# Kernel optimization log

Measured on AMD Instinct MI355X. Metric: run time of the kernel, lower is better.

Reference implementation:

```python
import jax, jax.numpy as jnp
import numpy as np

NUM_NODES = 100000
NUM_EDGES = 1600000
DIM = 64
NUM_LAYERS = 3


def setup_inputs() -> dict:
    key = jax.random.key(0)
    k1, k2 = jax.random.split(key)
    x = jax.random.normal(k1, (NUM_NODES, DIM), dtype=jnp.float32)
    adj_t = jax.random.randint(k2, (2, NUM_EDGES), 0, NUM_NODES, dtype=jnp.int64)
    return {"x": x, "adj_t": adj_t}


def reference(x, adj_t):
    n = x.shape[0]
    # undirected -> add reversed edges (adj_t_is_undirected=True path)
    edge_index = jnp.concatenate([adj_t, adj_t[::-1]], axis=1)  # [2, 2E]
    row, col = edge_index[0], edge_index[1]
    edge_weight = jnp.ones((row.shape[0],), dtype=x.dtype)
    # gcn_norm: D^-0.5 A D^-0.5 (degree computed by scatter over col)
    deg = jax.ops.segment_sum(edge_weight, col, num_segments=n)
    deg_inv_sqrt = jnp.where(deg > 0, jax.lax.rsqrt(deg), 0.0).astype(x.dtype)
    w = deg_inv_sqrt[row] * edge_weight * deg_inv_sqrt[col]  # [2E]
    outs = [x]
    for _ in range(NUM_LAYERS):
        # gather -> scale -> scatter_add (SpMM)
        msgs = w[:, None] * x[row]                     # [2E, D]
        x = jax.ops.segment_sum(msgs, col, num_segments=n)  # [N, D]
        outs.append(x)
    return jnp.mean(jnp.stack(outs), axis=0)
```

## Files before the change

### kernel.cpp

```cpp
#include <hip/hip_runtime.h>

#define DIM 64
#define SCAN_B 256
#define BKT_SHIFT 7
#define BKT_G 128
#define NBLK 256
#define HIST_B 1024

__device__ inline float blo(unsigned p) { return __uint_as_float(p << 16); }
__device__ inline float bhi(unsigned p) { return __uint_as_float(p & 0xffff0000u); }
__device__ inline unsigned bpack(float x, float y) {
    unsigned ux = __float_as_uint(x);
    unsigned uy = __float_as_uint(y);
    ux += 0x7fffu + ((ux >> 16) & 1u);
    uy += 0x7fffu + ((uy >> 16) & 1u);
    return (ux >> 16) | (uy & 0xffff0000u);
}

__global__ __launch_bounds__(HIST_B)
void hist_kernel(const int* __restrict__ adj, int E,
                 int* __restrict__ hist, int NB) {
    extern __shared__ int lh[];
    for (int g = threadIdx.x; g < NB; g += blockDim.x) lh[g] = 0;
    __syncthreads();
    for (int e = blockIdx.x * blockDim.x + threadIdx.x; e < E;
         e += NBLK * blockDim.x) {
        int a = adj[e];
        int b = adj[E + e];
        atomicAdd(&lh[a >> BKT_SHIFT], 1);
        atomicAdd(&lh[b >> BKT_SHIFT], 1);
    }
    __syncthreads();
    for (int g = threadIdx.x; g < NB; g += blockDim.x)
        hist[g * NBLK + blockIdx.x] = lh[g];
}

__global__ void scan_block_kernel(const int* __restrict__ src, int n,
                                  int* __restrict__ dst,
                                  int* __restrict__ blocksums) {
    __shared__ int tmp[SCAN_B];
    int i = blockIdx.x * SCAN_B + threadIdx.x;
    int v = (i < n) ? src[i] : 0;
    tmp[threadIdx.x] = v;
    __syncthreads();
    for (int off = 1; off < SCAN_B; off <<= 1) {
        int t = (threadIdx.x >= off) ? tmp[threadIdx.x - off] : 0;
        __syncthreads();
        tmp[threadIdx.x] += t;
        __syncthreads();
    }
    if (i < n) dst[i] = tmp[threadIdx.x] - v;
    if (threadIdx.x == SCAN_B - 1) blocksums[blockIdx.x] = tmp[SCAN_B - 1];
}

__global__ void scan_sums_kernel(int* __restrict__ blocksums, int nb) {
    __shared__ int tmp[1024];
    int v = (threadIdx.x < nb) ? blocksums[threadIdx.x] : 0;
    tmp[threadIdx.x] = v;
    __syncthreads();
    for (int off = 1; off < 1024; off <<= 1) {
        int t = (threadIdx.x >= off) ? tmp[threadIdx.x - off] : 0;
        __syncthreads();
        tmp[threadIdx.x] += t;
        __syncthreads();
    }
    if (threadIdx.x < nb) blocksums[threadIdx.x] = tmp[threadIdx.x] - v;
}

__global__ void scan_add_kernel(int* __restrict__ dst,
                                const int* __restrict__ blocksums,
                                int n, int total) {
    int i = blockIdx.x * blockDim.x + threadIdx.x;
    if (i < n) dst[i] += blocksums[i / SCAN_B];
    if (i == n) dst[n] = total;
}

__global__ __launch_bounds__(HIST_B)
void place_kernel(const int* __restrict__ adj, int E,
                  const int* __restrict__ hist_s,
                  unsigned* __restrict__ pairs, int NB) {
    extern __shared__ int cur[];
    for (int g = threadIdx.x; g < NB; g += blockDim.x)
        cur[g] = hist_s[g * NBLK + blockIdx.x];
    __syncthreads();
    for (int e = blockIdx.x * blockDim.x + threadIdx.x; e < E;
         e += NBLK * blockDim.x) {
        int a = adj[e];
        int b = adj[E + e];
        int pb = atomicAdd(&cur[b >> BKT_SHIFT], 1);
        pairs[pb] = ((unsigned)(b & (BKT_G - 1)) << 17) | (unsigned)a;
        int pa = atomicAdd(&cur[a >> BKT_SHIFT], 1);
        pairs[pa] = ((unsigned)(a & (BKT_G - 1)) << 17) | (unsigned)b;
    }
}

__global__ void pass2_build_kernel(const unsigned* __restrict__ pairs,
                                   const int* __restrict__ hist_s,
                                   const float4* __restrict__ x,
                                   int* __restrict__ csr_src,
                                   int* __restrict__ row_ptr,
                                   int* __restrict__ deg,
                                   float* __restrict__ dinv,
                                   uint4* __restrict__ xs0,
                                   int N, int total_adj) {
    __shared__ int cnt[BKT_G];
    __shared__ int pre[BKT_G];
    __shared__ int cur[BKT_G];
    __shared__ float dv[BKT_G];
    int g = blockIdx.x;
    int base = g << BKT_SHIFT;
    int off = hist_s[(size_t)g * NBLK];
    int offn = (g + 1 < gridDim.x) ? hist_s[(size_t)(g + 1) * NBLK] : total_adj;
    int m = offn - off;
    if (threadIdx.x < BKT_G) cnt[threadIdx.x] = 0;
    __syncthreads();
    for (int i = threadIdx.x; i < m; i += blockDim.x)
        atomicAdd(&cnt[pairs[off + i] >> 17], 1);
    __syncthreads();
    if (threadIdx.x < BKT_G) pre[threadIdx.x] = cnt[threadIdx.x];
    __syncthreads();
    for (int o = 1; o < BKT_G; o <<= 1) {
        int t = 0;
        if (threadIdx.x < BKT_G && threadIdx.x >= o) t = pre[threadIdx.x - o];
        __syncthreads();
        if (threadIdx.x < BKT_G) pre[threadIdx.x] += t;
        __syncthreads();
    }
    if (threadIdx.x < BKT_G) {
        int v = base + threadIdx.x;
        if (v < N) {
            int c = cnt[threadIdx.x];
            int start = off + pre[threadIdx.x] - c;
            float di = (c > 0) ? rsqrtf((float)c) : 0.0f;
            row_ptr[v] = start;
            deg[v] = c;
            dinv[v] = di;
            dv[threadIdx.x] = di;
            cur[threadIdx.x] = start;
        }
    }
    if (g == gridDim.x - 1 && threadIdx.x == 0) row_ptr[N] = total_adj;
    __syncthreads();
    for (int i = threadIdx.x; i < m; i += blockDim.x) {
        unsigned p = pairs[off + i];
        int dl  = (int)(p >> 17);
        int src = (int)(p & 0x1ffffu);
        int pos = atomicAdd(&cur[dl], 1);
        csr_src[pos] = src;
    }
    for (int w = threadIdx.x; w < BKT_G * 8; w += blockDim.x) {
        int vl = w >> 3, sub = w & 7;
        int v = base + vl;
        if (v < N) {
            float di = dv[vl];
            float4 xa = x[(size_t)v * 16 + sub * 2];
            float4 xb = x[(size_t)v * 16 + sub * 2 + 1];
            uint4 o;
            o.x = bpack(di * xa.x, di * xa.y);
            o.y = bpack(di * xa.z, di * xa.w);
            o.z = bpack(di * xb.x, di * xb.y);
            o.w = bpack(di * xb.z, di * xb.w);
            xs0[(size_t)v * 8 + sub] = o;
        }
    }
}

#define SPMM_ACCUM_BODY                                                        \
    int half = threadIdx.x & 31;                                               \
    int nb = half >> 3, sub = half & 7;                                        \
    int beg = row_ptr[v];                                                      \
    int end = row_ptr[v + 1];                                                  \
    int full = (end - beg) >> 4;                                               \
    float a0 = 0, a1 = 0, a2 = 0, a3 = 0, a4 = 0, a5 = 0, a6 = 0, a7 = 0;      \
    int j = beg;                                                               \
    int s0 = 0, s1 = 0, s2 = 0, s3 = 0;                                        \
    if (full > 0) {                                                            \
        int b = j + 4 * nb;                                                    \
        s0 = csr_src[b];     s1 = csr_src[b + 1];                              \
        s2 = csr_src[b + 2]; s3 = csr_src[b + 3];                              \
    }                                                                          \
    for (int it = 0; it < full; ++it) {                                        \
        int jn = j + 16;                                                       \
        int t0 = 0, t1 = 0, t2 = 0, t3 = 0;                                    \
        if (it + 1 < full) {                                                   \
            int b = jn + 4 * nb;                                               \
            t0 = csr_src[b];     t1 = csr_src[b + 1];                          \
            t2 = csr_src[b + 2]; t3 = csr_src[b + 3];                          \
        }                                                                      \
        uint4 p0 = xs_in[(size_t)s0 * 8 + sub];                                \
        uint4 p1 = xs_in[(size_t)s1 * 8 + sub];                                \
        uint4 p2 = xs_in[(size_t)s2 * 8 + sub];                                \
        uint4 p3 = xs_in[(size_t)s3 * 8 + sub];                                \
        a0 += (blo(p0.x) + blo(p1.x)) + (blo(p2.x) + blo(p3.x));               \
        a1 += (bhi(p0.x) + bhi(p1.x)) + (bhi(p2.x) + bhi(p3.x));               \
        a2 += (blo(p0.y) + blo(p1.y)) + (blo(p2.y) + blo(p3.y));               \
        a3 += (bhi(p0.y) + bhi(p1.y)) + (bhi(p2.y) + bhi(p3.y));               \
        a4 += (blo(p0.z) + blo(p1.z)) + (blo(p2.z) + blo(p3.z));               \
        a5 += (bhi(p0.z) + bhi(p1.z)) + (bhi(p2.z) + bhi(p3.z));               \
        a6 += (blo(p0.w) + blo(p1.w)) + (blo(p2.w) + blo(p3.w));               \
        a7 += (bhi(p0.w) + bhi(p1.w)) + (bhi(p2.w) + bhi(p3.w));               \
        s0 = t0; s1 = t1; s2 = t2; s3 = t3;                                    \
        j = jn;                                                                \
    }                                                                          \
    for (int idx = j + nb; idx < end; idx += 4) {                              \
        int s = csr_src[idx];                                                  \
        uint4 p = xs_in[(size_t)s * 8 + sub];                                  \
        a0 += blo(p.x); a1 += bhi(p.x);                                        \
        a2 += blo(p.y); a3 += bhi(p.y);                                        \
        a4 += blo(p.z); a5 += bhi(p.z);                                        \
        a6 += blo(p.w); a7 += bhi(p.w);                                        \
    }                                                                          \
    a0 += __shfl_xor(a0, 8);  a0 += __shfl_xor(a0, 16);                        \
    a1 += __shfl_xor(a1, 8);  a1 += __shfl_xor(a1, 16);                        \
    a2 += __shfl_xor(a2, 8);  a2 += __shfl_xor(a2, 16);                        \
    a3 += __shfl_xor(a3, 8);  a3 += __shfl_xor(a3, 16);                        \
    a4 += __shfl_xor(a4, 8);  a4 += __shfl_xor(a4, 16);                        \
    a5 += __shfl_xor(a5, 8);  a5 += __shfl_xor(a5, 16);                        \
    a6 += __shfl_xor(a6, 8);  a6 += __shfl_xor(a6, 16);                        \
    a7 += __shfl_xor(a7, 8);  a7 += __shfl_xor(a7, 16);

__global__ void spmm_bf16_kernel(const int* __restrict__ row_ptr,
                                 const int* __restrict__ csr_src,
                                 const float* __restrict__ dinv,
                                 const uint4* __restrict__ xs_in,
                                 uint4* __restrict__ xs_out, int N) {
    int t = blockIdx.x * blockDim.x + threadIdx.x;
    int v = t >> 5;
    if (v >= N) return;
    SPMM_ACCUM_BODY
    if (nb == 0) {
        float di = dinv[v];
        float d2 = di * di;
        uint4 o;
        o.x = bpack(d2 * a0, d2 * a1);
        o.y = bpack(d2 * a2, d2 * a3);
        o.z = bpack(d2 * a4, d2 * a5);
        o.w = bpack(d2 * a6, d2 * a7);
        xs_out[(size_t)v * 8 + sub] = o;
    }
}

__global__ void spmm_last_kernel(const int* __restrict__ row_ptr,
                                 const int* __restrict__ csr_src,
                                 const float* __restrict__ dinv,
                                 const int* __restrict__ deg,
                                 const uint4* __restrict__ xs_in,
                                 const uint4* __restrict__ xs1,
                                 const float4* __restrict__ x,
                                 float4* __restrict__ out, int N) {
    int t = blockIdx.x * blockDim.x + threadIdx.x;
    int v = t >> 5;
    if (v >= N) return;
    SPMM_ACCUM_BODY
    if (nb == 0) {
        float di = dinv[v];
        float rs = sqrtf((float)deg[v]);
        size_t idx = (size_t)v * 8 + sub;
        uint4 q1 = xs1[idx];
        uint4 q2 = xs_in[idx];
        float4 xa = x[(size_t)v * 16 + sub * 2];
        float4 xb = x[(size_t)v * 16 + sub * 2 + 1];
        float4 oa, ob;
        oa.x = 0.25f * (xa.x + rs * (blo(q1.x) + blo(q2.x)) + di * a0);
        oa.y = 0.25f * (xa.y + rs * (bhi(q1.x) + bhi(q2.x)) + di * a1);
        oa.z = 0.25f * (xa.z + rs * (blo(q1.y) + blo(q2.y)) + di * a2);
        oa.w = 0.25f * (xa.w + rs * (bhi(q1.y) + bhi(q2.y)) + di * a3);
        ob.x = 0.25f * (xb.x + rs * (blo(q1.z) + blo(q2.z)) + di * a4);
        ob.y = 0.25f * (xb.y + rs * (bhi(q1.z) + bhi(q2.z)) + di * a5);
        ob.z = 0.25f * (xb.z + rs * (blo(q1.w) + blo(q2.w)) + di * a6);
        ob.w = 0.25f * (xb.w + rs * (bhi(q1.w) + bhi(q2.w)) + di * a7);
        out[(size_t)v * 16 + sub * 2]     = oa;
        out[(size_t)v * 16 + sub * 2 + 1] = ob;
    }
}

extern "C" void kernel_launch(void* const* d_in, const int* in_sizes, int n_in,
                              void* d_out, int out_size, void* d_ws, size_t ws_size,
                              hipStream_t stream) {
    const float* x = (const float*)d_in[0];
    const int* adj = (const int*)d_in[1];
    float* out     = (float*)d_out;

    const int total_adj = in_sizes[1];
    const int E = total_adj / 2;
    const int N = in_sizes[0] / DIM;
    const int NB = (N + BKT_G - 1) / BKT_G;
    const int nhist = NB * NBLK;

    size_t BUF = (size_t)total_adj * 4;
    size_t xsb = (size_t)N * 32 * 4;
    if (xsb > BUF) BUF = xsb;
    BUF = (BUF + 255) & ~(size_t)255;

    char* ws = (char*)d_ws;
    int*      deg     = (int*)(ws);
    float*    dinv    = (float*)(ws + (size_t)512 * 1024);
    int*      row_ptr = (int*)(ws + (size_t)1024 * 1024);
    int*      bsums   = (int*)(ws + (size_t)1536 * 1024);
    int*      hist    = (int*)(ws + (size_t)1600 * 1024);
    int*      hist_s  = (int*)(ws + (size_t)2432 * 1024);
    char*     big     = ws + (size_t)3264 * 1024;
    int*      csr_src = (int*)(big);
    unsigned* pairs   = (unsigned*)(big + BUF);
    uint4*    xs0     = (uint4*)(big + 2 * BUF);
    uint4*    xs1     = (uint4*)(big + 3 * BUF);
    uint4*    xs2     = (uint4*)(big + 4 * BUF);

    const int B = 256;

    hist_kernel<<<NBLK, HIST_B, NB * sizeof(int), stream>>>(adj, E, hist, NB);

    const int nscan2 = (nhist + SCAN_B - 1) / SCAN_B;
    scan_block_kernel<<<nscan2, SCAN_B, 0, stream>>>(hist, nhist, hist_s, bsums);
    scan_sums_kernel<<<1, 1024, 0, stream>>>(bsums, nscan2);
    scan_add_kernel<<<(nhist + 1 + B - 1) / B, B, 0, stream>>>(hist_s, bsums, nhist, total_adj);

    place_kernel<<<NBLK, HIST_B, NB * sizeof(int), stream>>>(adj, E, hist_s, pairs, NB);

    pass2_build_kernel<<<NB, B, 0, stream>>>(pairs, hist_s, (const float4*)x,
                                             csr_src, row_ptr, deg, dinv,
                                             xs0, N, total_adj);

    const int nblocks32 = (int)(((long long)N * 32 + B - 1) / B);
    spmm_bf16_kernel<<<nblocks32, B, 0, stream>>>(row_ptr, csr_src, dinv, xs0, xs1, N);
    spmm_bf16_kernel<<<nblocks32, B, 0, stream>>>(row_ptr, csr_src, dinv, xs1, xs2, N);
    spmm_last_kernel<<<nblocks32, B, 0, stream>>>(row_ptr, csr_src, dinv, deg,
                                                  xs2, xs1, (const float4*)x,
                                                  (float4*)out, N);
}
```

Measured before the change: 300.9 us.

## Vectorize edge loads, replicate histograms, drop scan-add kernel, cache pairs in registers

The histogram and placement kernels now read edges as int4 and keep four replicated shared-memory histograms to spread atomic contention. The separate scan_add kernel is removed: since each bucket spans exactly NBLK=256 entries, one scan block per bucket, the block sums are the bucket base offsets and are added on the fly in place and build. The CSR build caches up to 20 pair records per thread in registers so the pairs array is not read twice. This costs more shared memory and register pressure, and the int4 path assumes adj is 16-byte aligned.

New measurement: 294.5 us. 1.02x faster.

```diff
diff --git a/kernel.cpp b/kernel.cpp
--- a/kernel.cpp
+++ b/kernel.cpp
@@ -6,6 +6,8 @@
 #define BKT_G 128
 #define NBLK 256
 #define HIST_B 1024
+#define NREP 4
+#define RCAP 20
 
 __device__ inline float blo(unsigned p) { return __uint_as_float(p << 16); }
 __device__ inline float bhi(unsigned p) { return __uint_as_float(p & 0xffff0000u); }
@@ -21,18 +23,35 @@
 void hist_kernel(const int* __restrict__ adj, int E,
                  int* __restrict__ hist, int NB) {
     extern __shared__ int lh[];
-    for (int g = threadIdx.x; g < NB; g += blockDim.x) lh[g] = 0;
-    __syncthreads();
-    for (int e = blockIdx.x * blockDim.x + threadIdx.x; e < E;
-         e += NBLK * blockDim.x) {
-        int a = adj[e];
-        int b = adj[E + e];
-        atomicAdd(&lh[a >> BKT_SHIFT], 1);
-        atomicAdd(&lh[b >> BKT_SHIFT], 1);
+    for (int g = threadIdx.x; g < NREP * NB; g += blockDim.x) lh[g] = 0;
+    __syncthreads();
+    const int rep = (threadIdx.x & (NREP - 1)) * NB;
+    const int n4 = E >> 2;
+    const int4* srcs = (const int4*)adj;
+    const int4* dsts = (const int4*)(adj + E);
+    for (int i = blockIdx.x * blockDim.x + threadIdx.x; i < n4;
+         i += NBLK * blockDim.x) {
+        int4 a = srcs[i];
+        int4 b = dsts[i];
+        atomicAdd(&lh[rep + (a.x >> BKT_SHIFT)], 1);
+        atomicAdd(&lh[rep + (a.y >> BKT_SHIFT)], 1);
+        atomicAdd(&lh[rep + (a.z >> BKT_SHIFT)], 1);
+        atomicAdd(&lh[rep + (a.w >> BKT_SHIFT)], 1);
+        atomicAdd(&lh[rep + (b.x >> BKT_SHIFT)], 1);
+        atomicAdd(&lh[rep + (b.y >> BKT_SHIFT)], 1);
+        atomicAdd(&lh[rep + (b.z >> BKT_SHIFT)], 1);
+        atomicAdd(&lh[rep + (b.w >> BKT_SHIFT)], 1);
+    }
+    if (blockIdx.x == 0) {
+        for (int e = (n4 << 2) + threadIdx.x; e < E; e += blockDim.x) {
+            atomicAdd(&lh[rep + (adj[e] >> BKT_SHIFT)], 1);
+            atomicAdd(&lh[rep + (adj[E + e] >> BKT_SHIFT)], 1);
+        }
     }
     __syncthreads();
     for (int g = threadIdx.x; g < NB; g += blockDim.x)
-        hist[g * NBLK + blockIdx.x] = lh[g];
+        hist[g * NBLK + blockIdx.x] =
+            lh[g] + lh[NB + g] + lh[2 * NB + g] + lh[3 * NB + g];
 }
 
 __global__ void scan_block_kernel(const int* __restrict__ src, int n,
@@ -67,55 +86,87 @@
     if (threadIdx.x < nb) blocksums[threadIdx.x] = tmp[threadIdx.x] - v;
 }
 
-__global__ void scan_add_kernel(int* __restrict__ dst,
-                                const int* __restrict__ blocksums,
-                                int n, int total) {
-    int i = blockIdx.x * blockDim.x + threadIdx.x;
-    if (i < n) dst[i] += blocksums[i / SCAN_B];
-    if (i == n) dst[n] = total;
-}
-
 __global__ __launch_bounds__(HIST_B)
 void place_kernel(const int* __restrict__ adj, int E,
                   const int* __restrict__ hist_s,
+                  const int* __restrict__ bsums,
                   unsigned* __restrict__ pairs, int NB) {
     extern __shared__ int cur[];
     for (int g = threadIdx.x; g < NB; g += blockDim.x)
-        cur[g] = hist_s[g * NBLK + blockIdx.x];
-    __syncthreads();
-    for (int e = blockIdx.x * blockDim.x + threadIdx.x; e < E;
-         e += NBLK * blockDim.x) {
-        int a = adj[e];
-        int b = adj[E + e];
-        int pb = atomicAdd(&cur[b >> BKT_SHIFT], 1);
-        pairs[pb] = ((unsigned)(b & (BKT_G - 1)) << 17) | (unsigned)a;
-        int pa = atomicAdd(&cur[a >> BKT_SHIFT], 1);
-        pairs[pa] = ((unsigned)(a & (BKT_G - 1)) << 17) | (unsigned)b;
-    }
-}
-
-__global__ void pass2_build_kernel(const unsigned* __restrict__ pairs,
-                                   const int* __restrict__ hist_s,
-                                   const float4* __restrict__ x,
-                                   int* __restrict__ csr_src,
-                                   int* __restrict__ row_ptr,
-                                   int* __restrict__ deg,
-                                   float* __restrict__ dinv,
-                                   uint4* __restrict__ xs0,
-                                   int N, int total_adj) {
+        cur[g] = hist_s[g * NBLK + blockIdx.x] + bsums[g];
+    __syncthreads();
+    const int n4 = E >> 2;
+    const int4* srcs = (const int4*)adj;
+    const int4* dsts = (const int4*)(adj + E);
+    for (int i = blockIdx.x * blockDim.x + threadIdx.x; i < n4;
+         i += NBLK * blockDim.x) {
+        int4 a = srcs[i];
+        int4 b = dsts[i];
+        int p;
+        p = atomicAdd(&cur[b.x >> BKT_SHIFT], 1);
+        pairs[p] = ((unsigned)(b.x & (BKT_G - 1)) << 17) | (unsigned)a.x;
+        p = atomicAdd(&cur[a.x >> BKT_SHIFT], 1);
+        pairs[p] = ((unsigned)(a.x & (BKT_G - 1)) << 17) | (unsigned)b.x;
+        p = atomicAdd(&cur[b.y >> BKT_SHIFT], 1);
+        pairs[p] = ((unsigned)(b.y & (BKT_G - 1)) << 17) | (unsigned)a.y;
+        p = atomicAdd(&cur[a.y >> BKT_SHIFT], 1);
+        pairs[p] = ((unsigned)(a.y & (BKT_G - 1)) << 17) | (unsigned)b.y;
+        p = atomicAdd(&cur[b.z >> BKT_SHIFT], 1);
+        pairs[p] = ((unsigned)(b.z & (BKT_G - 1)) << 17) | (unsigned)a.z;
+        p = atomicAdd(&cur[a.z >> BKT_SHIFT], 1);
+        pairs[p] = ((unsigned)(a.z & (BKT_G - 1)) << 17) | (unsigned)b.z;
+        p = atomicAdd(&cur[b.w >> BKT_SHIFT], 1);
+        pairs[p] = ((unsigned)(b.w & (BKT_G - 1)) << 17) | (unsigned)a.w;
+        p = atomicAdd(&cur[a.w >> BKT_SHIFT], 1);
+        pairs[p] = ((unsigned)(a.w & (BKT_G - 1)) << 17) | (unsigned)b.w;
+    }
+    if (blockIdx.x == 0) {
+        for (int e = (n4 << 2) + threadIdx.x; e < E; e += blockDim.x) {
+            int a = adj[e];
+            int b = adj[E + e];
+            int p1 = atomicAdd(&cur[b >> BKT_SHIFT], 1);
+            pairs[p1] = ((unsigned)(b & (BKT_G - 1)) << 17) | (unsigned)a;
+            int p2 = atomicAdd(&cur[a >> BKT_SHIFT], 1);
+            pairs[p2] = ((unsigned)(a & (BKT_G - 1)) << 17) | (unsigned)b;
+        }
+    }
+}
+
+__global__ __launch_bounds__(256)
+void pass2_build_kernel(const unsigned* __restrict__ pairs,
+                        const int* __restrict__ bsums,
+                        const float4* __restrict__ x,
+                        int* __restrict__ csr_src,
+                        int* __restrict__ row_ptr,
+                        int* __restrict__ deg,
+                        float* __restrict__ dinv,
+                        uint4* __restrict__ xs0,
+                        int N, int NB, int total_adj) {
     __shared__ int cnt[BKT_G];
     __shared__ int pre[BKT_G];
     __shared__ int cur[BKT_G];
     __shared__ float dv[BKT_G];
     int g = blockIdx.x;
     int base = g << BKT_SHIFT;
-    int off = hist_s[(size_t)g * NBLK];
-    int offn = (g + 1 < gridDim.x) ? hist_s[(size_t)(g + 1) * NBLK] : total_adj;
+    int off  = bsums[g];
+    int offn = (g + 1 < NB) ? bsums[g + 1] : total_adj;
     int m = offn - off;
     if (threadIdx.x < BKT_G) cnt[threadIdx.x] = 0;
     __syncthreads();
-    for (int i = threadIdx.x; i < m; i += blockDim.x)
-        atomicAdd(&cnt[pairs[off + i] >> 17], 1);
+    unsigned rec[RCAP];
+    int ibase = off + threadIdx.x;
+#pragma unroll
+    for (int k = 0; k < RCAP; ++k) {
+        int i = ibase + k * 256;
+        unsigned p = 0;
+        if (i < offn) {
+            p = pairs[i];
+            atomicAdd(&cnt[p >> 17], 1);
+        }
+        rec[k] = p;
+    }
+    for (int i = ibase + RCAP * 256; i < offn; i += 256)
+        atomicAdd(&cnt[pairs[i] >> 17], 1);
     __syncthreads();
     if (threadIdx.x < BKT_G) pre[threadIdx.x] = cnt[threadIdx.x];
     __syncthreads();
@@ -139,14 +190,21 @@
             cur[threadIdx.x] = start;
         }
     }
-    if (g == gridDim.x - 1 && threadIdx.x == 0) row_ptr[N] = total_adj;
-    __syncthreads();
-    for (int i = threadIdx.x; i < m; i += blockDim.x) {
-        unsigned p = pairs[off + i];
-        int dl  = (int)(p >> 17);
-        int src = (int)(p & 0x1ffffu);
-        int pos = atomicAdd(&cur[dl], 1);
-        csr_src[pos] = src;
+    if (g == NB - 1 && threadIdx.x == 0) row_ptr[N] = total_adj;
+    __syncthreads();
+#pragma unroll
+    for (int k = 0; k < RCAP; ++k) {
+        int i = ibase + k * 256;
+        if (i < offn) {
+            unsigned p = rec[k];
+            int pos = atomicAdd(&cur[p >> 17], 1);
+            csr_src[pos] = (int)(p & 0x1ffffu);
+        }
+    }
+    for (int i = ibase + RCAP * 256; i < offn; i += 256) {
+        unsigned p = pairs[i];
+        int pos = atomicAdd(&cur[p >> 17], 1);
+        csr_src[pos] = (int)(p & 0x1ffffu);
     }
     for (int w = threadIdx.x; w < BKT_G * 8; w += blockDim.x) {
         int vl = w >> 3, sub = w & 7;
@@ -308,18 +366,18 @@
 
     const int B = 256;
 
-    hist_kernel<<<NBLK, HIST_B, NB * sizeof(int), stream>>>(adj, E, hist, NB);
+    hist_kernel<<<NBLK, HIST_B, NREP * NB * sizeof(int), stream>>>(adj, E, hist, NB);
 
     const int nscan2 = (nhist + SCAN_B - 1) / SCAN_B;
     scan_block_kernel<<<nscan2, SCAN_B, 0, stream>>>(hist, nhist, hist_s, bsums);
     scan_sums_kernel<<<1, 1024, 0, stream>>>(bsums, nscan2);
-    scan_add_kernel<<<(nhist + 1 + B - 1) / B, B, 0, stream>>>(hist_s, bsums, nhist, total_adj);
-
-    place_kernel<<<NBLK, HIST_B, NB * sizeof(int), stream>>>(adj, E, hist_s, pairs, NB);
-
-    pass2_build_kernel<<<NB, B, 0, stream>>>(pairs, hist_s, (const float4*)x,
+
+    place_kernel<<<NBLK, HIST_B, NB * sizeof(int), stream>>>(adj, E, hist_s,
+                                                             bsums, pairs, NB);
+
+    pass2_build_kernel<<<NB, B, 0, stream>>>(pairs, bsums, (const float4*)x,
                                              csr_src, row_ptr, deg, dinv,
-                                             xs0, N, total_adj);
+                                             xs0, N, NB, total_adj);
 
     const int nblocks32 = (int)(((long long)N * 32 + B - 1) / B);
     spmm_bf16_kernel<<<nblocks32, B, 0, stream>>>(row_ptr, csr_src, dinv, xs0, xs1, N);
```
